# Kernel optimization log

Hardware: AMD Instinct MI355X
Metric: run time of the kernel (lower is better)

The kernel has to match this reference:

```python
import jax, jax.numpy as jnp
import numpy as np

N = 100000   # nodes
E = 1600000  # edges
D = 64       # in_feats
H = 512      # hidden_dim
O = 64       # out_feats
K = 3        # hops
LN_EPS = 1e-5


def setup_inputs() -> dict:
    key = jax.random.key(0)
    ks = jax.random.split(key, 10)
    x = jax.random.normal(ks[0], (N, D), dtype=jnp.float32)
    edge_index = jax.random.randint(ks[1], (2, E), 0, N, dtype=jnp.int64)
    # SAGEConv lin_l weights (root_weight=False, bias=False): K stacked [D, D]
    w_prop = jax.random.normal(ks[2], (K, D, D), dtype=jnp.float32) / np.sqrt(D)
    lin1_w = jax.random.normal(ks[3], ((K + 1) * D, H), dtype=jnp.float32) / np.sqrt((K + 1) * D)
    lin1_b = jnp.zeros((H,), dtype=jnp.float32)
    ln_gamma = jnp.ones((H,), dtype=jnp.float32)
    ln_beta = jnp.zeros((H,), dtype=jnp.float32)
    lin2_w = jax.random.normal(ks[4], (H, O), dtype=jnp.float32) / np.sqrt(H)
    lin2_b = jnp.zeros((O,), dtype=jnp.float32)
    return {
        "x": x, "edge_index": edge_index, "w_prop": w_prop,
        "lin1_w": lin1_w, "lin1_b": lin1_b,
        "ln_gamma": ln_gamma, "ln_beta": ln_beta,
        "lin2_w": lin2_w, "lin2_b": lin2_b,
    }


def _sage_mean(h, src, dst, w):
    # mean-aggregate neighbor features at dst, then linear (no root, no bias)
    msg_sum = jax.ops.segment_sum(h[src], dst, num_segments=N)       # [N, D]
    deg = jax.ops.segment_sum(jnp.ones((E,), h.dtype), dst, num_segments=N)
    agg = msg_sum / jnp.maximum(deg, 1.0)[:, None]
    return agg @ w


def reference(x, edge_index, w_prop, lin1_w, lin1_b, ln_gamma, ln_beta, lin2_w, lin2_b):
    src, dst = edge_index[0], edge_index[1]
    zs = [x]
    curr = x
    for i in range(K):
        curr = _sage_mean(curr, src, dst, w_prop[i])
        zs.append(curr)
    h = jnp.concatenate(zs, axis=1)          # [N, (K+1)*D]
    h = h @ lin1_w + lin1_b                   # [N, H]
    mu = jnp.mean(h, axis=-1, keepdims=True)
    var = jnp.var(h, axis=-1, keepdims=True)
    h = (h - mu) * jax.lax.rsqrt(var + LN_EPS) * ln_gamma + ln_beta
    h = jax.nn.relu(h)
    # dropout is identity in eval mode (training=False)
    return h @ lin2_w + lin2_b                # [N, O]
```

## Files before the change

kernel.cpp:

```cpp
#include <hip/hip_runtime.h>

constexpr int NN = 100000;
constexpr int NE = 1600000;
constexpr int NBUK = 196;
constexpr int ECAP = 10240;
constexpr int CHUNK = 6250;
constexpr int NPT = 13;

typedef __attribute__((ext_vector_type(8))) short bf16x8;
typedef __attribute__((ext_vector_type(4))) float f32x4;

__device__ inline ushort f2b(float f){
  uint u = __float_as_uint(f);
  uint r = (u + 0x7FFFu + ((u >> 16) & 1u)) >> 16;
  return (ushort)r;
}
__device__ inline float b2f(ushort u){
  uint v = ((uint)u) << 16;
  return __uint_as_float(v);
}

template<int CTRL>
__device__ inline float dpp_xadd(float v){
  int j = __builtin_amdgcn_update_dpp(0, __float_as_int(v), CTRL, 0xF, 0xF, true);
  return v + __int_as_float(j);
}
__device__ inline float red16(float v){
  v = dpp_xadd<0xB1>(v);
  v = dpp_xadd<0x4E>(v);
  v = dpp_xadd<0x141>(v);
  v = dpp_xadd<0x140>(v);
  return v;
}

__global__ __launch_bounds__(512) void k_part1(const int* __restrict__ srcA,
                                               const int* __restrict__ dstA,
                                               int* __restrict__ bukcur,
                                               int* __restrict__ ebuf,
                                               const float* __restrict__ x,
                                               ushort* __restrict__ xb){
  __shared__ int stage[CHUNK];
  __shared__ unsigned char bstage[CHUNK];
  __shared__ int hist[256];
  __shared__ int lofs[256];
  __shared__ int lcur[NBUK];
  __shared__ int basebuf[NBUK];
  int t = threadIdx.x;
  int cbase = blockIdx.x * CHUNK;

  if (t < 256) hist[t] = 0;
  if (t < NBUK) lcur[t] = 0;
  __syncthreads();

  int pk[NPT], bb[NPT];
  #pragma unroll
  for (int j = 0; j < NPT; ++j){
    int i = t + j*512;
    bb[j] = -1;
    if (i < CHUNK){
      int e = cbase + i;
      int d = dstA[e];
      bb[j] = d >> 9;
      pk[j] = (srcA[e] << 9) | (d & 511);
      atomicAdd(&hist[bb[j]], 1);
    }
  }
  __syncthreads();

  int v = (t < 256) ? hist[t] : 0;
  if (t < 256) lofs[t] = v;
  __syncthreads();
  #pragma unroll
  for (int off = 1; off < 256; off <<= 1){
    int tv = (t < 256 && t >= off) ? lofs[t-off] : 0;
    __syncthreads();
    if (t < 256) lofs[t] += tv;
    __syncthreads();
  }
  if (t < 256) lofs[t] -= v;
  if (t < NBUK) basebuf[t] = atomicAdd(&bukcur[t], v);
  __syncthreads();

  #pragma unroll
  for (int j = 0; j < NPT; ++j){
    if (bb[j] >= 0){
      int p = atomicAdd(&lcur[bb[j]], 1);
      int slot = lofs[bb[j]] + p;
      stage[slot] = pk[j];
      bstage[slot] = (unsigned char)bb[j];
    }
  }
  __syncthreads();

  for (int i = t; i < CHUNK; i += 512){
    int b = bstage[i];
    int j = i - lofs[b];
    int pos = basebuf[b] + j;
    if (pos < ECAP) ebuf[b*ECAP + pos] = stage[i];
  }

  for (int i = blockIdx.x*512 + t; i < NN*16; i += 256*512){
    float4 vv = ((const float4*)x)[i];
    ushort4 o;
    o.x = f2b(vv.x); o.y = f2b(vv.y); o.z = f2b(vv.z); o.w = f2b(vv.w);
    ((ushort4*)xb)[i] = o;
  }
}

__global__ __launch_bounds__(512) void k_bfinal(const int* __restrict__ ebuf,
                                                const int* __restrict__ bukcur,
                                                int* __restrict__ rbeg,
                                                int* __restrict__ degA,
                                                int* __restrict__ csr){
  __shared__ int lcnt[512];
  __shared__ int lscan[512];
  __shared__ int lcur[512];
  int b = blockIdx.x, t = threadIdx.x;
  int cnt = bukcur[b]; if (cnt > ECAP) cnt = ECAP;
  int base = b*ECAP, gbase = b*ECAP;

  lcnt[t] = 0; lcur[t] = 0;
  __syncthreads();
  for (int i = t; i < cnt; i += 512) atomicAdd(&lcnt[ebuf[base+i] & 511], 1);
  __syncthreads();
  int v = lcnt[t];
  lscan[t] = v; __syncthreads();
  #pragma unroll
  for (int off = 1; off < 512; off <<= 1){
    int tv = (t >= off) ? lscan[t-off] : 0;
    __syncthreads();
    lscan[t] += tv;
    __syncthreads();
  }
  int excl = lscan[t] - v;
  lcnt[t] = excl;
  int node = b*512 + t;
  if (node < NN){ rbeg[node] = gbase + excl; degA[node] = v; }
  __syncthreads();
  for (int i = t; i < cnt; i += 512){
    int p = ebuf[base+i];
    int d = p & 511;
    int pos = atomicAdd(&lcur[d], 1);
    csr[gbase + lcnt[d] + pos] = p >> 9;
  }
}

__global__ __launch_bounds__(256) void k_wprep(const float* __restrict__ Wp,
                                               const float* __restrict__ W1,
                                               const float* __restrict__ W2,
                                               ushort* __restrict__ W1t,
                                               ushort* __restrict__ W2t){
  int b = blockIdx.x, t = threadIdx.x;
  if (b >= 512){
    int col = b - 512;
    for (int k = t; k < 512; k += 256)
      W2t[col*512 + k] = f2b(W2[(size_t)k*64 + col]);
    return;
  }
  __shared__ float sA[4096];
  __shared__ float sB[4096];
  __shared__ float sV2[4096];
  __shared__ float col[256];
  __shared__ float u[64];

  for (int i = t; i < 4096; i += 256){ sA[i] = Wp[i]; sB[i] = Wp[4096+i]; }
  __syncthreads();
  for (int i = t; i < 4096; i += 256){
    int r = i >> 6, c = i & 63; float s = 0.f;
    #pragma unroll 8
    for (int j = 0; j < 64; ++j) s += sA[r*64+j]*sB[j*64+c];
    sV2[i] = s;
  }
  __syncthreads();
  for (int i = t; i < 4096; i += 256) sB[i] = Wp[8192+i];
  col[t] = W1[(size_t)t*512 + b];
  __syncthreads();
  if (t < 64){
    float s = 0.f;
    #pragma unroll 8
    for (int j = 0; j < 64; ++j) s += sB[t*64+j]*col[192+j];
    u[t] = s;
  }
  __syncthreads();

  int p = t >> 6, i2 = t & 63;
  float s;
  if (p == 0) s = col[t];
  else if (p == 1){
    s = 0.f;
    #pragma unroll 8
    for (int j = 0; j < 64; ++j) s += sA[i2*64+j]*col[64+j];
  } else if (p == 2){
    s = 0.f;
    #pragma unroll 8
    for (int j = 0; j < 64; ++j) s += sV2[i2*64+j]*col[128+j];
  } else {
    s = 0.f;
    #pragma unroll 8
    for (int j = 0; j < 64; ++j) s += sV2[i2*64+j]*u[j];
  }
  W1t[b*256 + t] = f2b(s);
}

__global__ void k_aggb(const ushort* __restrict__ hb, const int* __restrict__ rbeg,
                       const int* __restrict__ degA, const int* __restrict__ csr,
                       ushort* __restrict__ yb){
  int lane = threadIdx.x & 63;
  int wv = threadIdx.x >> 6;
  int f = lane & 7, s = lane >> 3;
  int n = blockIdx.x*32 + wv*8 + s;
  int beg = rbeg[n], dg = degA[n];
  float a[8] = {};
  int i = 0;
  for (; i + 4 <= dg; i += 4){
    int i0 = csr[beg+i], i1 = csr[beg+i+1], i2 = csr[beg+i+2], i3 = csr[beg+i+3];
    bf16x8 v0 = *(const bf16x8*)(hb + (size_t)i0*64 + f*8);
    bf16x8 v1 = *(const bf16x8*)(hb + (size_t)i1*64 + f*8);
    bf16x8 v2 = *(const bf16x8*)(hb + (size_t)i2*64 + f*8);
    bf16x8 v3 = *(const bf16x8*)(hb + (size_t)i3*64 + f*8);
    #pragma unroll
    for (int j = 0; j < 8; ++j)
      a[j] += (b2f((ushort)v0[j]) + b2f((ushort)v1[j]))
            + (b2f((ushort)v2[j]) + b2f((ushort)v3[j]));
  }
  for (; i < dg; ++i){
    int i0 = csr[beg+i];
    bf16x8 v = *(const bf16x8*)(hb + (size_t)i0*64 + f*8);
    #pragma unroll
    for (int j = 0; j < 8; ++j) a[j] += b2f((ushort)v[j]);
  }
  float inv = 1.f / fmaxf((float)dg, 1.f);
  bf16x8 o;
  #pragma unroll
  for (int j = 0; j < 8; ++j) o[j] = (short)f2b(a[j]*inv);
  *(bf16x8*)(yb + (size_t)n*64 + f*8) = o;
}

__global__ __launch_bounds__(512, 4) void k_mlp(
    const ushort* __restrict__ cat0,
    const ushort* __restrict__ W1t, const float* __restrict__ b1,
    const float* __restrict__ gamma, const float* __restrict__ beta,
    const ushort* __restrict__ W2t, const float* __restrict__ b2,
    float* __restrict__ out){
  constexpr size_t PSTR = 6400000;
  __shared__ char lbuf[65536];
  __shared__ float2 s_pair[8][64];
  __shared__ float2 s_stat2[64];

  int tid = threadIdx.x;
  int lane = tid & 63, wv = tid >> 6;
  int l15 = lane & 15, l4 = lane >> 4;

  int bid = blockIdx.x;
  {
    constexpr int NB = 1563, q = NB/8, r = NB%8;
    int xcd = bid & 7, idx = bid >> 3;
    bid = (xcd < r ? xcd*(q+1) : r*(q+1) + (xcd-r)*q) + idx;
  }
  int nbase = bid * 64;

  #pragma unroll
  for (int i = 0; i < 4; ++i){
    int dest = (wv*4 + i)*1024 + lane*16;
    int row = dest >> 9;
    int kbyte = (dest & 511) ^ ((row & 7) << 4);
    const ushort* src = cat0 + (size_t)(kbyte >> 7)*PSTR
                             + (size_t)(nbase + row)*64 + ((kbyte & 127) >> 1);
    __builtin_amdgcn_global_load_lds(
        (const __attribute__((address_space(1))) void*)src,
        (__attribute__((address_space(3))) void*)(lbuf + (wv*4 + i)*1024),
        16, 0, 0);
  }
  __syncthreads();

  #define LOADA(kb, d)                                                          \
    { _Pragma("unroll")                                                         \
      for (int rt = 0; rt < 4; ++rt){                                           \
        int row_ = rt*16 + l15;                                                 \
        d[rt] = *(const bf16x8*)(lbuf + row_*512 +                              \
                 (((kb)*64 + l4*16) ^ ((row_ & 7) << 4)));                      \
      } }
  #define LOADB(kb, d)                                                          \
    { _Pragma("unroll")                                                         \
      for (int ci = 0; ci < 4; ++ci)                                            \
        d[ci] = *(const bf16x8*)(W1t + (size_t)(wv*64 + ci*16 + l15)*256 +      \
                                 (kb)*32 + l4*8); }

  f32x4 acc[4][4] = {};
  bf16x8 a[4], b[2][4];
  LOADB(0, b[0]);
  #pragma unroll
  for (int kb = 0; kb < 8; ++kb){
    int cur = kb & 1, nxt = cur ^ 1;
    if (kb < 7) LOADB(kb+1, b[nxt]);
    LOADA(kb, a);
    __builtin_amdgcn_s_setprio(1);
    #pragma unroll
    for (int rt = 0; rt < 4; ++rt)
      #pragma unroll
      for (int ci = 0; ci < 4; ++ci)
        acc[rt][ci] = __builtin_amdgcn_mfma_f32_16x16x32_bf16(a[rt], b[cur][ci], acc[rt][ci], 0, 0, 0);
    __builtin_amdgcn_s_setprio(0);
  }

  float bcol[4], gcol[4], ecol[4];
  #pragma unroll
  for (int ci = 0; ci < 4; ++ci){
    int col = wv*64 + ci*16 + l15;
    bcol[ci] = b1[col]; gcol[ci] = gamma[col]; ecol[ci] = beta[col];
  }
  #pragma unroll
  for (int rt = 0; rt < 4; ++rt)
    #pragma unroll
    for (int ci = 0; ci < 4; ++ci)
      #pragma unroll
      for (int r = 0; r < 4; ++r)
        acc[rt][ci][r] += bcol[ci];

  #pragma unroll
  for (int rt = 0; rt < 4; ++rt){
    #pragma unroll
    for (int r = 0; r < 4; ++r){
      float s = 0.f, q = 0.f;
      #pragma unroll
      for (int ci = 0; ci < 4; ++ci){
        float v = acc[rt][ci][r];
        s += v; q += v*v;
      }
      s = red16(s);
      q = red16(q);
      if (l15 == 0) s_pair[wv][rt*16 + l4*4 + r] = make_float2(s, q);
    }
  }
  __syncthreads();

  if (tid < 64){
    float s = 0.f, q = 0.f;
    #pragma unroll
    for (int w = 0; w < 8; ++w){ float2 p = s_pair[w][tid]; s += p.x; q += p.y; }
    float mu = s * (1.f/512.f);
    float var = q * (1.f/512.f) - mu*mu;
    s_stat2[tid] = make_float2(mu, rsqrtf(var + 1e-5f));
  }
  __syncthreads();

  #pragma unroll
  for (int rt = 0; rt < 4; ++rt){
    #pragma unroll
    for (int r = 0; r < 4; ++r){
      int row = rt*16 + l4*4 + r;
      float2 st = s_stat2[row];
      #pragma unroll
      for (int ci = 0; ci < 4; ++ci){
        float hv = fmaxf((acc[rt][ci][r] - st.x)*st.y*gcol[ci] + ecol[ci], 0.f);
        int col = wv*64 + ci*16 + l15;
        *((ushort*)(lbuf + row*1024 + ((col*2) ^ ((row & 7) << 4)))) = f2b(hv);
      }
    }
  }
  __syncthreads();

  #define LOADH(kb, d)                                                          \
    { _Pragma("unroll")                                                         \
      for (int t = 0; t < 2; ++t){                                              \
        int row_ = (rtb + t)*16 + l15;                                          \
        d[t] = *(const bf16x8*)(lbuf + row_*1024 +                              \
                 (((kb)*64 + l4*16) ^ ((row_ & 7) << 4)));                      \
      } }

  int ct = wv >> 1;
  int rtb = (wv & 1) * 2;
  f32x4 acc2[2] = {};
  const ushort* w2base = W2t + (size_t)(ct*16 + l15)*512 + l4*8;
  bf16x8 hb2[2][2], w2f[2];
  w2f[0] = *(const bf16x8*)(w2base);
  LOADH(0, hb2[0]);
  #pragma unroll
  for (int kb = 0; kb < 16; ++kb){
    int cur = kb & 1, nxt = cur ^ 1;
    if (kb < 15){
      w2f[nxt] = *(const bf16x8*)(w2base + (kb+1)*32);
      LOADH(kb+1, hb2[nxt]);
    }
    __builtin_amdgcn_s_setprio(1);
    acc2[0] = __builtin_amdgcn_mfma_f32_16x16x32_bf16(hb2[cur][0], w2f[cur], acc2[0], 0, 0, 0);
    acc2[1] = __builtin_amdgcn_mfma_f32_16x16x32_bf16(hb2[cur][1], w2f[cur], acc2[1], 0, 0, 0);
    __builtin_amdgcn_s_setprio(0);
  }

  float b2v = b2[ct*16 + l15];
  #pragma unroll
  for (int t = 0; t < 2; ++t){
    #pragma unroll
    for (int r = 0; r < 4; ++r){
      int row = (rtb + t)*16 + l4*4 + r;
      if (nbase + row < NN)
        out[(size_t)(nbase + row)*64 + ct*16 + l15] = acc2[t][r] + b2v;
    }
  }
  #undef LOADA
  #undef LOADB
  #undef LOADH
}

extern "C" void kernel_launch(void* const* d_in, const int* in_sizes, int n_in,
                              void* d_out, int out_size, void* d_ws, size_t ws_size,
                              hipStream_t stream){
  const float* x     = (const float*)d_in[0];
  const int*   eidx  = (const int*)d_in[1];
  const float* wprop = (const float*)d_in[2];
  const float* W1    = (const float*)d_in[3];
  const float* b1    = (const float*)d_in[4];
  const float* gamma = (const float*)d_in[5];
  const float* beta  = (const float*)d_in[6];
  const float* W2    = (const float*)d_in[7];
  const float* b2    = (const float*)d_in[8];
  float* out = (float*)d_out;
  const int* srcA = eidx;
  const int* dstA = eidx + NE;

  char* ws = (char*)d_ws;
  int*    rbeg   = (int*)(ws);
  int*    degA   = (int*)(ws +      400384);
  ushort* W1t    = (ushort*)(ws +   800768);
  ushort* W2t    = (ushort*)(ws +  1062912);
  int*    bukcur = (int*)(ws +     1128448);
  int*    csr    = (int*)(ws +     1129472);
  int*    ebuf   = (int*)(ws +     9157632);
  ushort* xb     = (ushort*)(ws + 17185792);
  ushort* y1     = (ushort*)(ws + 29985792);
  ushort* y2     = (ushort*)(ws + 42785792);
  ushort* y3     = (ushort*)(ws + 55585792);

  hipMemsetAsync(bukcur, 0, NBUK*sizeof(int), stream);
  k_part1<<<256, 512, 0, stream>>>(srcA, dstA, bukcur, ebuf, x, xb);
  k_bfinal<<<NBUK, 512, 0, stream>>>(ebuf, bukcur, rbeg, degA, csr);

  k_wprep<<<576, 256, 0, stream>>>(wprop, W1, W2, W1t, W2t);

  k_aggb<<<3125, 256, 0, stream>>>(xb, rbeg, degA, csr, y1);
  k_aggb<<<3125, 256, 0, stream>>>(y1, rbeg, degA, csr, y2);
  k_aggb<<<3125, 256, 0, stream>>>(y2, rbeg, degA, csr, y3);

  k_mlp<<<1563, 512, 0, stream>>>(xb, W1t, b1, gamma, beta, W2t, b2, out);
}
```

Before: 244.2 us.

## Fuse third-hop aggregation into MLP kernel prologue, writing directly to LDS

Drops the third aggregation launch and computes the hop-3 mean aggregate inside the MLP kernel, storing the bf16 result straight into the swizzled LDS tile instead of loading y3 from global memory. This removes one kernel launch and the global write and re-read of y3. In exchange, the MLP prologue now does irregular gather work, which may delay the GEMM phase and raise register pressure in a kernel with launch bounds of 512 threads and 4 blocks.

```diff
diff --git a/kernel.cpp b/kernel.cpp
--- a/kernel.cpp
+++ b/kernel.cpp
@@ -238,6 +238,8 @@
 
 __global__ __launch_bounds__(512, 4) void k_mlp(
     const ushort* __restrict__ cat0,
+    const int* __restrict__ rbeg, const int* __restrict__ degA,
+    const int* __restrict__ csr,
     const ushort* __restrict__ W1t, const float* __restrict__ b1,
     const float* __restrict__ gamma, const float* __restrict__ beta,
     const ushort* __restrict__ W2t, const float* __restrict__ b2,
@@ -261,15 +263,51 @@
 
   #pragma unroll
   for (int i = 0; i < 4; ++i){
-    int dest = (wv*4 + i)*1024 + lane*16;
-    int row = dest >> 9;
-    int kbyte = (dest & 511) ^ ((row & 7) << 4);
-    const ushort* src = cat0 + (size_t)(kbyte >> 7)*PSTR
-                             + (size_t)(nbase + row)*64 + ((kbyte & 127) >> 1);
-    __builtin_amdgcn_global_load_lds(
-        (const __attribute__((address_space(1))) void*)src,
-        (__attribute__((address_space(3))) void*)(lbuf + (wv*4 + i)*1024),
-        16, 0, 0);
+    if ((lane & 31) < 24){
+      int dest = (wv*4 + i)*1024 + lane*16;
+      int row = dest >> 9;
+      int kbyte = (dest & 511) ^ ((row & 7) << 4);
+      const ushort* src = cat0 + (size_t)(kbyte >> 7)*PSTR
+                               + (size_t)(nbase + row)*64 + ((kbyte & 127) >> 1);
+      __builtin_amdgcn_global_load_lds(
+          (const __attribute__((address_space(1))) void*)src,
+          (__attribute__((address_space(3))) void*)(lbuf + (wv*4 + i)*1024),
+          16, 0, 0);
+    }
+  }
+
+  {
+    const ushort* y2 = cat0 + 2*PSTR;
+    int node = tid >> 3;
+    int f = tid & 7;
+    int gnode = nbase + node;
+    int beg = 0, dg = 0;
+    if (gnode < NN){ beg = rbeg[gnode]; dg = degA[gnode]; }
+    float a[8] = {};
+    int i = 0;
+    for (; i + 4 <= dg; i += 4){
+      int i0 = csr[beg+i], i1 = csr[beg+i+1], i2 = csr[beg+i+2], i3 = csr[beg+i+3];
+      bf16x8 v0 = *(const bf16x8*)(y2 + (size_t)i0*64 + f*8);
+      bf16x8 v1 = *(const bf16x8*)(y2 + (size_t)i1*64 + f*8);
+      bf16x8 v2 = *(const bf16x8*)(y2 + (size_t)i2*64 + f*8);
+      bf16x8 v3 = *(const bf16x8*)(y2 + (size_t)i3*64 + f*8);
+      #pragma unroll
+      for (int j = 0; j < 8; ++j)
+        a[j] += (b2f((ushort)v0[j]) + b2f((ushort)v1[j]))
+              + (b2f((ushort)v2[j]) + b2f((ushort)v3[j]));
+    }
+    for (; i < dg; ++i){
+      int i0 = csr[beg+i];
+      bf16x8 v = *(const bf16x8*)(y2 + (size_t)i0*64 + f*8);
+      #pragma unroll
+      for (int j = 0; j < 8; ++j) a[j] += b2f((ushort)v[j]);
+    }
+    float inv = 1.f / fmaxf((float)dg, 1.f);
+    bf16x8 o;
+    #pragma unroll
+    for (int j = 0; j < 8; ++j) o[j] = (short)f2b(a[j]*inv);
+    int kbyte = (384 + f*16) ^ ((node & 7) << 4);
+    *(bf16x8*)(lbuf + node*512 + kbyte) = o;
   }
   __syncthreads();
 
@@ -430,7 +468,6 @@
   ushort* xb     = (ushort*)(ws + 17185792);
   ushort* y1     = (ushort*)(ws + 29985792);
   ushort* y2     = (ushort*)(ws + 42785792);
-  ushort* y3     = (ushort*)(ws + 55585792);
 
   hipMemsetAsync(bukcur, 0, NBUK*sizeof(int), stream);
   k_part1<<<256, 512, 0, stream>>>(srcA, dstA, bukcur, ebuf, x, xb);
@@ -440,7 +477,6 @@
 
   k_aggb<<<3125, 256, 0, stream>>>(xb, rbeg, degA, csr, y1);
   k_aggb<<<3125, 256, 0, stream>>>(y1, rbeg, degA, csr, y2);
-  k_aggb<<<3125, 256, 0, stream>>>(y2, rbeg, degA, csr, y3);
-
-  k_mlp<<<1563, 512, 0, stream>>>(xb, W1t, b1, gamma, beta, W2t, b2, out);
-}
+
+  k_mlp<<<1563, 512, 0, stream>>>(xb, rbeg, degA, csr, W1t, b1, gamma, beta, W2t, b2, out);
+}
```

Result: no change. 245.4 us (+0.5%).
